# Performance work log

Measured on AMD Instinct MI355X. Metric: run time of the kernel, lower is better.

Reference implementation:

```python
import jax, jax.numpy as jnp
import numpy as np

N_NODES = 100000
N_EDGES = 1600000
DIMS = [128, 128, 128, 64]  # in, h1, h2, out


def setup_inputs() -> dict:
    key = jax.random.key(0)
    ks = jax.random.split(key, 12)
    inp = {
        "x": jax.random.normal(ks[0], (N_NODES, DIMS[0]), dtype=jnp.float32),
        "edge_index": jax.random.randint(ks[1], (2, N_EDGES), 0, N_NODES, dtype=jnp.int64),
        "edge_weights": jax.random.uniform(ks[2], (N_EDGES,), dtype=jnp.float32),
    }
    for i in range(3):
        inp[f"W{i+1}"] = jax.random.normal(ks[3 + 2 * i], (DIMS[i], DIMS[i + 1]), dtype=jnp.float32) * 0.05
        inp[f"b{i+1}"] = jax.random.normal(ks[4 + 2 * i], (DIMS[i + 1],), dtype=jnp.float32) * 0.01
    return inp


def gcn_conv(x, src, dst, w, W, b, n_nodes):
    # PyG GCNConv: linear transform, symmetric gcn_norm with self-loops (weight 1), scatter-add, bias.
    xw = x @ W                                            # [N, out]
    deg = jax.ops.segment_sum(w, dst, num_segments=n_nodes) + 1.0  # self-loop weight 1
    dinv = jnp.where(deg > 0, jax.lax.rsqrt(deg), 0.0)    # deg^{-1/2}
    norm = dinv[src] * w * dinv[dst]                      # [E]
    out = jax.ops.segment_sum(norm[:, None] * xw[src], dst, num_segments=n_nodes)
    out = out + (dinv * dinv)[:, None] * xw               # self-loop message
    return out + b


def reference(x, edge_index, edge_weights, W1, b1, W2, b2, W3, b3):
    src, dst = edge_index[0], edge_index[1]
    n = x.shape[0]
    # layer 1: GCNConv -> dropout(p=0) -> relu
    h = jax.nn.relu(gcn_conv(x, src, dst, edge_weights, W1, b1, n))
    # layer 2
    h = jax.nn.relu(gcn_conv(h, src, dst, edge_weights, W2, b2, n))
    # layer 3: activation 'none' -> Identity
    h = gcn_conv(h, src, dst, edge_weights, W3, b3, n)
    return h
```

## Files before the change

### kernel.cpp

```cpp
#include <hip/hip_runtime.h>
#include <hip/hip_fp16.h>
#include <math.h>


typedef __bf16 bf16x8 __attribute__((ext_vector_type(8)));
typedef float f32x4 __attribute__((ext_vector_type(4)));

union BF8 {
  unsigned short u[8];
  uint4 q;
  bf16x8 v;
};

union H8 {
  uint4 q;
  __half2 h2[4];
};

__device__ __forceinline__ unsigned short rne_bf16(float f) {
  unsigned u = __float_as_uint(f);
  u += 0x7fff + ((u >> 16) & 1);
  return (unsigned short)(u >> 16);
}
__device__ __forceinline__ float bf16_to_f(unsigned short h) {
  return __uint_as_float((unsigned)h << 16);
}

__device__ __forceinline__ void gemm_body_slice(const float* __restrict__ A,
    const float* __restrict__ W, int ldw, int col0,
    unsigned short* __restrict__ Ch, int ldc, int M, int bid) {
  constexpr int NF = 4;
  __shared__ __align__(16) unsigned short WT[2][64][128];
  const int t = threadIdx.x;
#pragma unroll
  for (int it = 0; it < 4; ++it) {
    int n = t & 63;
    int kc = it * 4 + (t >> 6);
    int k0 = kc * 8;
    BF8 hh, ll;
#pragma unroll
    for (int j = 0; j < 8; ++j) {
      float w = W[(size_t)(k0 + j) * ldw + col0 + n];
      unsigned short hb = rne_bf16(w);
      hh.u[j] = hb;
      ll.u[j] = rne_bf16(w - bf16_to_f(hb));
    }
    int kk = k0 ^ ((n & 7) << 3);
    *(uint4*)&WT[0][n][kk] = hh.q;
    *(uint4*)&WT[1][n][kk] = ll.q;
  }
  __syncthreads();

  const int wv = t >> 6;
  const int l = t & 63;
  const int lr = l & 15;
  const int lg = l >> 4;
  const int arow_i = bid * 64 + wv * 16 + lr;
  const bool rv = arow_i < M;
  const float* arow = A + (size_t)arow_i * 128;

  f32x4 acc[NF] = {};
  float4 p0 = make_float4(0.f, 0.f, 0.f, 0.f), p1 = p0;
  if (rv) {
    p0 = *(const float4*)&arow[lg * 8];
    p1 = *(const float4*)&arow[lg * 8 + 4];
  }
#pragma unroll 1
  for (int ks = 0; ks < 4; ++ks) {
    int nkb = ((ks < 3) ? (ks + 1) * 32 : ks * 32) + lg * 8;
    float4 q0 = make_float4(0.f, 0.f, 0.f, 0.f), q1 = q0;
    if (rv) {
      q0 = *(const float4*)&arow[nkb];
      q1 = *(const float4*)&arow[nkb + 4];
    }
    float av[8] = {p0.x, p0.y, p0.z, p0.w, p1.x, p1.y, p1.z, p1.w};
    BF8 ah, al;
#pragma unroll
    for (int j = 0; j < 8; ++j) {
      unsigned short hb = rne_bf16(av[j]);
      ah.u[j] = hb;
      al.u[j] = rne_bf16(av[j] - bf16_to_f(hb));
    }
    int kidx = ks * 32 + lg * 8;
    BF8 bh[NF], bl[NF];
#pragma unroll
    for (int nf = 0; nf < NF; ++nf) {
      int n = nf * 16 + lr;
      int kk = kidx ^ ((n & 7) << 3);
      bh[nf].q = *(const uint4*)&WT[0][n][kk];
      bl[nf].q = *(const uint4*)&WT[1][n][kk];
    }
#pragma unroll
    for (int nf = 0; nf < NF; ++nf) {
      acc[nf] = __builtin_amdgcn_mfma_f32_16x16x32_bf16(ah.v, bh[nf].v, acc[nf], 0, 0, 0);
      acc[nf] = __builtin_amdgcn_mfma_f32_16x16x32_bf16(al.v, bh[nf].v, acc[nf], 0, 0, 0);
      acc[nf] = __builtin_amdgcn_mfma_f32_16x16x32_bf16(ah.v, bl[nf].v, acc[nf], 0, 0, 0);
    }
    p0 = q0; p1 = q1;
  }
  const int orow0 = bid * 64 + wv * 16 + lg * 4;
#pragma unroll
  for (int j = 0; j < 4; ++j) {
    int orow = orow0 + j;
    if (orow < M) {
      unsigned short* hr = Ch + (size_t)orow * ldc + col0;
#pragma unroll
      for (int nf = 0; nf < NF; ++nf)
        hr[nf * 16 + lr] = __half_as_ushort(__float2half(acc[nf][j]));
    }
  }
}

__global__ __launch_bounds__(256) void pre_gemm_fused_kernel(
    const float* __restrict__ x, const float* __restrict__ W1,
    unsigned short* __restrict__ Ch, int M,
    const int* __restrict__ ei, const float* __restrict__ ew,
    unsigned long long* __restrict__ packed, int* __restrict__ rank,
    int E, int edgeBlocks) {
  if ((int)blockIdx.x < edgeBlocks) {
    int e = blockIdx.x * 256 + threadIdx.x;
    if (e >= E) return;
    int d = ei[E + e];
    unsigned wfix = (unsigned)__float2uint_rn(ew[e] * 16777216.0f);
    unsigned long long inc = (1ULL << 32) | (unsigned long long)wfix;
    unsigned long long old = atomicAdd(&packed[d], inc);
    rank[e] = (int)(old >> 32);
  } else {
    int g = blockIdx.x - edgeBlocks;
    gemm_body_slice(x, W1, 128, (g & 1) * 64, Ch, 128, M, g >> 1);
  }
}

template <int NCOL>
__global__ __launch_bounds__(256) void gemm_mfma_kernel(
    const unsigned short* __restrict__ Ah, const float* __restrict__ W,
    unsigned short* __restrict__ Ch, int M) {
  constexpr int NF = NCOL / 16;
  __shared__ __align__(16) unsigned short WT[2][NCOL][128];
  const int t = threadIdx.x;
  constexpr int KC_PER_IT = 256 / NCOL;
#pragma unroll
  for (int it = 0; it < 16 / KC_PER_IT; ++it) {
    int n = t % NCOL;
    int kc = it * KC_PER_IT + t / NCOL;
    int k0 = kc * 8;
    BF8 hh, ll;
#pragma unroll
    for (int j = 0; j < 8; ++j) {
      float w = W[(size_t)(k0 + j) * NCOL + n];
      unsigned short hb = rne_bf16(w);
      hh.u[j] = hb;
      ll.u[j] = rne_bf16(w - bf16_to_f(hb));
    }
    int kk = k0 ^ ((n & 7) << 3);
    *(uint4*)&WT[0][n][kk] = hh.q;
    *(uint4*)&WT[1][n][kk] = ll.q;
  }
  __syncthreads();

  const int wv = t >> 6;
  const int l = t & 63;
  const int lr = l & 15;
  const int lg = l >> 4;
  const int arow_i = blockIdx.x * 64 + wv * 16 + lr;
  const bool rv = arow_i < M;
  const unsigned short* arowh = Ah + (size_t)arow_i * 128;

  f32x4 acc[NF] = {};
  uint4 ph = make_uint4(0, 0, 0, 0);
  if (rv) ph = *(const uint4*)&arowh[lg * 8];
#pragma unroll 1
  for (int ks = 0; ks < 4; ++ks) {
    int nkb = ((ks < 3) ? (ks + 1) * 32 : ks * 32) + lg * 8;
    uint4 qh = make_uint4(0, 0, 0, 0);
    if (rv) qh = *(const uint4*)&arowh[nkb];
    float av[8];
    {
      H8 uu; uu.q = ph;
#pragma unroll
      for (int j = 0; j < 4; ++j) {
        float2 f = __half22float2(uu.h2[j]);
        av[j * 2] = f.x; av[j * 2 + 1] = f.y;
      }
    }
    BF8 ah, al;
#pragma unroll
    for (int j = 0; j < 8; ++j) {
      unsigned short hb = rne_bf16(av[j]);
      ah.u[j] = hb;
      al.u[j] = rne_bf16(av[j] - bf16_to_f(hb));
    }
    int kidx = ks * 32 + lg * 8;
    BF8 bh[NF], bl[NF];
#pragma unroll
    for (int nf = 0; nf < NF; ++nf) {
      int n = nf * 16 + lr;
      int kk = kidx ^ ((n & 7) << 3);
      bh[nf].q = *(const uint4*)&WT[0][n][kk];
      bl[nf].q = *(const uint4*)&WT[1][n][kk];
    }
#pragma unroll
    for (int nf = 0; nf < NF; ++nf) {
      acc[nf] = __builtin_amdgcn_mfma_f32_16x16x32_bf16(ah.v, bh[nf].v, acc[nf], 0, 0, 0);
      acc[nf] = __builtin_amdgcn_mfma_f32_16x16x32_bf16(al.v, bh[nf].v, acc[nf], 0, 0, 0);
      acc[nf] = __builtin_amdgcn_mfma_f32_16x16x32_bf16(ah.v, bl[nf].v, acc[nf], 0, 0, 0);
    }
    ph = qh;
  }
  const int orow0 = blockIdx.x * 64 + wv * 16 + lg * 4;
#pragma unroll
  for (int j = 0; j < 4; ++j) {
    int orow = orow0 + j;
    if (orow < M) {
      unsigned short* hr = Ch + (size_t)orow * NCOL;
#pragma unroll
      for (int nf = 0; nf < NF; ++nf)
        hr[nf * 16 + lr] = __half_as_ushort(__float2half(acc[nf][j]));
    }
  }
}

__global__ __launch_bounds__(1024) void scanA(const unsigned long long* __restrict__ packed,
    int* __restrict__ row_ptr, int* __restrict__ partials,
    float* __restrict__ dinv, int n) {
  __shared__ int sd[1024];
  int t = threadIdx.x;
  int i = blockIdx.x * 1024 + t;
  unsigned long long pv = (i < n) ? packed[i] : 0ULL;
  int v = (int)(pv >> 32);
  if (i < n) {
    float deg = 1.0f + (float)(unsigned)(pv & 0xffffffffULL) * (1.0f / 16777216.0f);
    dinv[i] = 1.0f / sqrtf(deg);
  }
  sd[t] = v;
  __syncthreads();
  for (int off = 1; off < 1024; off <<= 1) {
    int u = (t >= off) ? sd[t - off] : 0;
    __syncthreads();
    sd[t] += u;
    __syncthreads();
  }
  int incl = sd[t];
  if (i < n) row_ptr[i] = incl - v;
  if (t == 1023) partials[blockIdx.x] = incl;
}

__global__ __launch_bounds__(128) void scanB(int* partials, int nb) {
  __shared__ int sd[128];
  int t = threadIdx.x;
  int v = (t < nb) ? partials[t] : 0;
  sd[t] = v;
  __syncthreads();
  for (int off = 1; off < 128; off <<= 1) {
    int u = (t >= off) ? sd[t - off] : 0;
    __syncthreads();
    sd[t] += u;
    __syncthreads();
  }
  int incl = sd[t];
  partials[t] = incl - v;
  if (t == nb - 1) partials[255] = incl;
}

__global__ __launch_bounds__(1024) void scanC(int* row_ptr, const int* __restrict__ partials, int n) {
  int i = blockIdx.x * 1024 + threadIdx.x;
  if (i < n) row_ptr[i] += partials[blockIdx.x];
  if (i == 0) row_ptr[n] = partials[255];
}

__global__ __launch_bounds__(256) void fill_kernel(const int* __restrict__ ei,
    const float* __restrict__ ew, const float* __restrict__ dinv,
    const int* __restrict__ row_ptr, const int* __restrict__ rank,
    int2* __restrict__ epair, int E) {
  int e = blockIdx.x * 256 + threadIdx.x;
  if (e >= E) return;
  int s = ei[e], d = ei[E + e];
  float nw = dinv[s] * ew[e] * dinv[d];
  int p = row_ptr[d] + rank[e];
  epair[p] = make_int2(s, __float_as_int(nw));
}

template <int F, bool RELU, bool OUTF16>
__global__ __launch_bounds__(256) void agg_kernel(const unsigned short* __restrict__ xwh,
    const int* __restrict__ row_ptr, const int2* __restrict__ epair,
    const float* __restrict__ dinv, const float* __restrict__ bias,
    void* __restrict__ out, int Nn) {
  constexpr int LPN = F / 8;
  int t = blockIdx.x * 256 + threadIdx.x;
  int node = t / LPN;
  int lane = t % LPN;
  if (node >= Nn) return;
  const uint4* xh = (const uint4*)xwh;
  int start = row_ptr[node];
  int end = row_ptr[node + 1];
  float a0[8] = {}, a1[8] = {};
  int p = start;
  for (; p + 4 <= end; p += 4) {
    int2 e0 = epair[p];
    int2 e1 = epair[p + 1];
    int2 e2 = epair[p + 2];
    int2 e3 = epair[p + 3];
    H8 u0, u1, u2, u3;
    u0.q = xh[(size_t)e0.x * LPN + lane];
    u1.q = xh[(size_t)e1.x * LPN + lane];
    u2.q = xh[(size_t)e2.x * LPN + lane];
    u3.q = xh[(size_t)e3.x * LPN + lane];
    float n0 = __int_as_float(e0.y), n1 = __int_as_float(e1.y);
    float n2 = __int_as_float(e2.y), n3 = __int_as_float(e3.y);
#pragma unroll
    for (int j = 0; j < 4; ++j) {
      float2 f0 = __half22float2(u0.h2[j]);
      float2 f1 = __half22float2(u1.h2[j]);
      float2 f2 = __half22float2(u2.h2[j]);
      float2 f3 = __half22float2(u3.h2[j]);
      a0[j * 2]     = fmaf(n0, f0.x, a0[j * 2]);
      a0[j * 2 + 1] = fmaf(n0, f0.y, a0[j * 2 + 1]);
      a1[j * 2]     = fmaf(n1, f1.x, a1[j * 2]);
      a1[j * 2 + 1] = fmaf(n1, f1.y, a1[j * 2 + 1]);
      a0[j * 2]     = fmaf(n2, f2.x, a0[j * 2]);
      a0[j * 2 + 1] = fmaf(n2, f2.y, a0[j * 2 + 1]);
      a1[j * 2]     = fmaf(n3, f3.x, a1[j * 2]);
      a1[j * 2 + 1] = fmaf(n3, f3.y, a1[j * 2 + 1]);
    }
  }
  for (; p < end; ++p) {
    int2 pr = epair[p];
    float nw = __int_as_float(pr.y);
    H8 u; u.q = xh[(size_t)pr.x * LPN + lane];
#pragma unroll
    for (int j = 0; j < 4; ++j) {
      float2 f = __half22float2(u.h2[j]);
      a0[j * 2]     = fmaf(nw, f.x, a0[j * 2]);
      a0[j * 2 + 1] = fmaf(nw, f.y, a0[j * 2 + 1]);
    }
  }
  float di = dinv[node];
  float sw = di * di;
  H8 su; su.q = xh[(size_t)node * LPN + lane];
#pragma unroll
  for (int j = 0; j < 4; ++j) {
    float2 f = __half22float2(su.h2[j]);
    a0[j * 2]     = fmaf(sw, f.x, a0[j * 2]);
    a0[j * 2 + 1] = fmaf(sw, f.y, a0[j * 2 + 1]);
  }
  float4 b0 = ((const float4*)bias)[lane * 2];
  float4 b1 = ((const float4*)bias)[lane * 2 + 1];
  float o[8];
  o[0] = a0[0] + a1[0] + b0.x; o[1] = a0[1] + a1[1] + b0.y;
  o[2] = a0[2] + a1[2] + b0.z; o[3] = a0[3] + a1[3] + b0.w;
  o[4] = a0[4] + a1[4] + b1.x; o[5] = a0[5] + a1[5] + b1.y;
  o[6] = a0[6] + a1[6] + b1.z; o[7] = a0[7] + a1[7] + b1.w;
  if (RELU) {
#pragma unroll
    for (int j = 0; j < 8; ++j) o[j] = fmaxf(o[j], 0.f);
  }
  if constexpr (OUTF16) {
    H8 w;
#pragma unroll
    for (int j = 0; j < 4; ++j)
      w.h2[j] = __float22half2_rn(make_float2(o[j * 2], o[j * 2 + 1]));
    ((uint4*)out)[(size_t)node * LPN + lane] = w.q;
  } else {
    float4* of = (float4*)out + (size_t)node * LPN * 2 + lane * 2;
    of[0] = make_float4(o[0], o[1], o[2], o[3]);
    of[1] = make_float4(o[4], o[5], o[6], o[7]);
  }
}

extern "C" void kernel_launch(void* const* d_in, const int* in_sizes, int n_in,
                              void* d_out, int out_size, void* d_ws, size_t ws_size,
                              hipStream_t stream) {
  const float* x  = (const float*)d_in[0];
  const int*   ei = (const int*)d_in[1];
  const float* ew = (const float*)d_in[2];
  const float* W1 = (const float*)d_in[3];
  const float* b1 = (const float*)d_in[4];
  const float* W2 = (const float*)d_in[5];
  const float* b2 = (const float*)d_in[6];
  const float* W3 = (const float*)d_in[7];
  const float* b3 = (const float*)d_in[8];

  const int N = in_sizes[0] / 128;
  const int E = in_sizes[2];

  char* ws = (char*)d_ws;
  size_t off = 0;
  auto carve = [&](size_t bytes) -> void* {
    void* p = ws + off;
    off += (bytes + 255) & ~(size_t)255;
    return p;
  };
  unsigned long long* packed = (unsigned long long*)carve((size_t)N * 8);
  int*   rank    = (int*)carve((size_t)E * 4);
  float* dinv    = (float*)carve((size_t)N * 4);
  int*   row_ptr = (int*)carve((size_t)(N + 1) * 4);
  int*   parts   = (int*)carve(256 * 4);
  int2*  epair   = (int2*)carve((size_t)E * 8);
  unsigned short* bufH = (unsigned short*)carve((size_t)N * 128 * 2);
  unsigned short* bufI = (unsigned short*)carve((size_t)N * 128 * 2);
  (void)ws_size; (void)n_in; (void)out_size;

  const int nThreads = 256;
  int gE  = (E + nThreads - 1) / nThreads;
  int nb  = (N + 1023) / 1024;
  const int gMM = (N + 63) / 64;
  int gAgg128 = (N * 16 + nThreads - 1) / nThreads;
  int gAgg64  = (N * 8 + nThreads - 1) / nThreads;

  hipMemsetAsync(packed, 0, (size_t)N * 8, stream);
  pre_gemm_fused_kernel<<<gE + 2 * gMM, nThreads, 0, stream>>>(
      x, W1, bufH, N, ei, ew, packed, rank, E, gE);

  scanA<<<nb, 1024, 0, stream>>>(packed, row_ptr, parts, dinv, N);
  scanB<<<1, 128, 0, stream>>>(parts, nb);
  scanC<<<nb, 1024, 0, stream>>>(row_ptr, parts, N);
  fill_kernel<<<gE, nThreads, 0, stream>>>(ei, ew, dinv, row_ptr, rank, epair, E);

  agg_kernel<128, true, true><<<gAgg128, nThreads, 0, stream>>>(bufH, row_ptr, epair, dinv, b1, bufI, N);

  gemm_mfma_kernel<128><<<gMM, nThreads, 0, stream>>>(bufI, W2, bufH, N);
  agg_kernel<128, true, true><<<gAgg128, nThreads, 0, stream>>>(bufH, row_ptr, epair, dinv, b2, bufI, N);

  gemm_mfma_kernel<64><<<gMM, nThreads, 0, stream>>>(bufI, W3, bufH, N);
  agg_kernel<64, false, false><<<gAgg64, nThreads, 0, stream>>>(bufH, row_ptr, epair, dinv, b3, d_out, N);
}
```

Before: 341.4 us.

## Process two 16-row tiles per wave in MFMA GEMMs to reuse B fragments

```diff
diff --git a/kernel.cpp b/kernel.cpp
--- a/kernel.cpp
+++ b/kernel.cpp
@@ -24,6 +24,15 @@
 }
 __device__ __forceinline__ float bf16_to_f(unsigned short h) {
   return __uint_as_float((unsigned)h << 16);
+}
+
+__device__ __forceinline__ void split_f32_to_bf(const float* av, BF8& ah, BF8& al) {
+#pragma unroll
+  for (int j = 0; j < 8; ++j) {
+    unsigned short hb = rne_bf16(av[j]);
+    ah.u[j] = hb;
+    al.u[j] = rne_bf16(av[j] - bf16_to_f(hb));
+  }
 }
 
 __device__ __forceinline__ void gemm_body_slice(const float* __restrict__ A,
@@ -55,58 +64,60 @@
   const int l = t & 63;
   const int lr = l & 15;
   const int lg = l >> 4;
-  const int arow_i = bid * 64 + wv * 16 + lr;
-  const bool rv = arow_i < M;
-  const float* arow = A + (size_t)arow_i * 128;
-
-  f32x4 acc[NF] = {};
-  float4 p0 = make_float4(0.f, 0.f, 0.f, 0.f), p1 = p0;
-  if (rv) {
-    p0 = *(const float4*)&arow[lg * 8];
-    p1 = *(const float4*)&arow[lg * 8 + 4];
-  }
+  const int r0 = bid * 128 + wv * 32 + lr;
+  const int r1 = r0 + 16;
+  const bool v0 = r0 < M, v1 = r1 < M;
+  const float* a0p = A + (size_t)r0 * 128;
+  const float* a1p = A + (size_t)r1 * 128;
+
+  f32x4 acc0[NF] = {}, acc1[NF] = {};
+  float4 p00 = make_float4(0.f, 0.f, 0.f, 0.f), p01 = p00, p10 = p00, p11 = p00;
+  if (v0) { p00 = *(const float4*)&a0p[lg * 8]; p01 = *(const float4*)&a0p[lg * 8 + 4]; }
+  if (v1) { p10 = *(const float4*)&a1p[lg * 8]; p11 = *(const float4*)&a1p[lg * 8 + 4]; }
 #pragma unroll 1
   for (int ks = 0; ks < 4; ++ks) {
     int nkb = ((ks < 3) ? (ks + 1) * 32 : ks * 32) + lg * 8;
-    float4 q0 = make_float4(0.f, 0.f, 0.f, 0.f), q1 = q0;
-    if (rv) {
-      q0 = *(const float4*)&arow[nkb];
-      q1 = *(const float4*)&arow[nkb + 4];
-    }
-    float av[8] = {p0.x, p0.y, p0.z, p0.w, p1.x, p1.y, p1.z, p1.w};
-    BF8 ah, al;
-#pragma unroll
-    for (int j = 0; j < 8; ++j) {
-      unsigned short hb = rne_bf16(av[j]);
-      ah.u[j] = hb;
-      al.u[j] = rne_bf16(av[j] - bf16_to_f(hb));
-    }
+    float4 q00 = make_float4(0.f, 0.f, 0.f, 0.f), q01 = q00, q10 = q00, q11 = q00;
+    if (v0) { q00 = *(const float4*)&a0p[nkb]; q01 = *(const float4*)&a0p[nkb + 4]; }
+    if (v1) { q10 = *(const float4*)&a1p[nkb]; q11 = *(const float4*)&a1p[nkb + 4]; }
+    float av0[8] = {p00.x, p00.y, p00.z, p00.w, p01.x, p01.y, p01.z, p01.w};
+    float av1[8] = {p10.x, p10.y, p10.z, p10.w, p11.x, p11.y, p11.z, p11.w};
+    BF8 ah0, al0, ah1, al1;
+    split_f32_to_bf(av0, ah0, al0);
+    split_f32_to_bf(av1, ah1, al1);
     int kidx = ks * 32 + lg * 8;
-    BF8 bh[NF], bl[NF];
 #pragma unroll
     for (int nf = 0; nf < NF; ++nf) {
       int n = nf * 16 + lr;
       int kk = kidx ^ ((n & 7) << 3);
-      bh[nf].q = *(const uint4*)&WT[0][n][kk];
-      bl[nf].q = *(const uint4*)&WT[1][n][kk];
-    }
-#pragma unroll
-    for (int nf = 0; nf < NF; ++nf) {
-      acc[nf] = __builtin_amdgcn_mfma_f32_16x16x32_bf16(ah.v, bh[nf].v, acc[nf], 0, 0, 0);
-      acc[nf] = __builtin_amdgcn_mfma_f32_16x16x32_bf16(al.v, bh[nf].v, acc[nf], 0, 0, 0);
-      acc[nf] = __builtin_amdgcn_mfma_f32_16x16x32_bf16(ah.v, bl[nf].v, acc[nf], 0, 0, 0);
-    }
-    p0 = q0; p1 = q1;
-  }
-  const int orow0 = bid * 64 + wv * 16 + lg * 4;
+      BF8 bh, bl;
+      bh.q = *(const uint4*)&WT[0][n][kk];
+      bl.q = *(const uint4*)&WT[1][n][kk];
+      acc0[nf] = __builtin_amdgcn_mfma_f32_16x16x32_bf16(ah0.v, bh.v, acc0[nf], 0, 0, 0);
+      acc0[nf] = __builtin_amdgcn_mfma_f32_16x16x32_bf16(al0.v, bh.v, acc0[nf], 0, 0, 0);
+      acc0[nf] = __builtin_amdgcn_mfma_f32_16x16x32_bf16(ah0.v, bl.v, acc0[nf], 0, 0, 0);
+      acc1[nf] = __builtin_amdgcn_mfma_f32_16x16x32_bf16(ah1.v, bh.v, acc1[nf], 0, 0, 0);
+      acc1[nf] = __builtin_amdgcn_mfma_f32_16x16x32_bf16(al1.v, bh.v, acc1[nf], 0, 0, 0);
+      acc1[nf] = __builtin_amdgcn_mfma_f32_16x16x32_bf16(ah1.v, bl.v, acc1[nf], 0, 0, 0);
+    }
+    p00 = q00; p01 = q01; p10 = q10; p11 = q11;
+  }
+  const int ob = bid * 128 + wv * 32 + lg * 4;
 #pragma unroll
   for (int j = 0; j < 4; ++j) {
-    int orow = orow0 + j;
+    int orow = ob + j;
     if (orow < M) {
       unsigned short* hr = Ch + (size_t)orow * ldc + col0;
 #pragma unroll
       for (int nf = 0; nf < NF; ++nf)
-        hr[nf * 16 + lr] = __half_as_ushort(__float2half(acc[nf][j]));
+        hr[nf * 16 + lr] = __half_as_ushort(__float2half(acc0[nf][j]));
+    }
+    int orow1 = ob + 16 + j;
+    if (orow1 < M) {
+      unsigned short* hr = Ch + (size_t)orow1 * ldc + col0;
+#pragma unroll
+      for (int nf = 0; nf < NF; ++nf)
+        hr[nf * 16 + lr] = __half_as_ushort(__float2half(acc1[nf][j]));
     }
   }
 }
@@ -162,60 +173,73 @@
   const int l = t & 63;
   const int lr = l & 15;
   const int lg = l >> 4;
-  const int arow_i = blockIdx.x * 64 + wv * 16 + lr;
-  const bool rv = arow_i < M;
-  const unsigned short* arowh = Ah + (size_t)arow_i * 128;
-
-  f32x4 acc[NF] = {};
-  uint4 ph = make_uint4(0, 0, 0, 0);
-  if (rv) ph = *(const uint4*)&arowh[lg * 8];
+  const int r0 = blockIdx.x * 128 + wv * 32 + lr;
+  const int r1 = r0 + 16;
+  const bool v0 = r0 < M, v1 = r1 < M;
+  const unsigned short* a0p = Ah + (size_t)r0 * 128;
+  const unsigned short* a1p = Ah + (size_t)r1 * 128;
+
+  f32x4 acc0[NF] = {}, acc1[NF] = {};
+  uint4 ph0 = make_uint4(0, 0, 0, 0), ph1 = ph0;
+  if (v0) ph0 = *(const uint4*)&a0p[lg * 8];
+  if (v1) ph1 = *(const uint4*)&a1p[lg * 8];
 #pragma unroll 1
   for (int ks = 0; ks < 4; ++ks) {
     int nkb = ((ks < 3) ? (ks + 1) * 32 : ks * 32) + lg * 8;
-    uint4 qh = make_uint4(0, 0, 0, 0);
-    if (rv) qh = *(const uint4*)&arowh[nkb];
-    float av[8];
+    uint4 qh0 = make_uint4(0, 0, 0, 0), qh1 = qh0;
+    if (v0) qh0 = *(const uint4*)&a0p[nkb];
+    if (v1) qh1 = *(const uint4*)&a1p[nkb];
+    float av0[8], av1[8];
     {
-      H8 uu; uu.q = ph;
+      H8 uu; uu.q = ph0;
 #pragma unroll
       for (int j = 0; j < 4; ++j) {
         float2 f = __half22float2(uu.h2[j]);
-        av[j * 2] = f.x; av[j * 2 + 1] = f.y;
+        av0[j * 2] = f.x; av0[j * 2 + 1] = f.y;
       }
-    }
-    BF8 ah, al;
-#pragma unroll
-    for (int j = 0; j < 8; ++j) {
-      unsigned short hb = rne_bf16(av[j]);
-      ah.u[j] = hb;
-      al.u[j] = rne_bf16(av[j] - bf16_to_f(hb));
-    }
+      uu.q = ph1;
+#pragma unroll
+      for (int j = 0; j < 4; ++j) {
+        float2 f = __half22float2(uu.h2[j]);
+        av1[j * 2] = f.x; av1[j * 2 + 1] = f.y;
+      }
+    }
+    BF8 ah0, al0, ah1, al1;
+    split_f32_to_bf(av0, ah0, al0);
+    split_f32_to_bf(av1, ah1, al1);
     int kidx = ks * 32 + lg * 8;
-    BF8 bh[NF], bl[NF];
 #pragma unroll
     for (int nf = 0; nf < NF; ++nf) {
       int n = nf * 16 + lr;
       int kk = kidx ^ ((n & 7) << 3);
-      bh[nf].q = *(const uint4*)&WT[0][n][kk];
-      bl[nf].q = *(const uint4*)&WT[1][n][kk];
-    }
-#pragma unroll
-    for (int nf = 0; nf < NF; ++nf) {
-      acc[nf] = __builtin_amdgcn_mfma_f32_16x16x32_bf16(ah.v, bh[nf].v, acc[nf], 0, 0, 0);
-      acc[nf] = __builtin_amdgcn_mfma_f32_16x16x32_bf16(al.v, bh[nf].v, acc[nf], 0, 0, 0);
-      acc[nf] = __builtin_amdgcn_mfma_f32_16x16x32_bf16(ah.v, bl[nf].v, acc[nf], 0, 0, 0);
-    }
-    ph = qh;
-  }
-  const int orow0 = blockIdx.x * 64 + wv * 16 + lg * 4;
+      BF8 bh, bl;
+      bh.q = *(const uint4*)&WT[0][n][kk];
+      bl.q = *(const uint4*)&WT[1][n][kk];
+      acc0[nf] = __builtin_amdgcn_mfma_f32_16x16x32_bf16(ah0.v, bh.v, acc0[nf], 0, 0, 0);
+      acc0[nf] = __builtin_amdgcn_mfma_f32_16x16x32_bf16(al0.v, bh.v, acc0[nf], 0, 0, 0);
+      acc0[nf] = __builtin_amdgcn_mfma_f32_16x16x32_bf16(ah0.v, bl.v, acc0[nf], 0, 0, 0);
+      acc1[nf] = __builtin_amdgcn_mfma_f32_16x16x32_bf16(ah1.v, bh.v, acc1[nf], 0, 0, 0);
+      acc1[nf] = __builtin_amdgcn_mfma_f32_16x16x32_bf16(al1.v, bh.v, acc1[nf], 0, 0, 0);
+      acc1[nf] = __builtin_amdgcn_mfma_f32_16x16x32_bf16(ah1.v, bl.v, acc1[nf], 0, 0, 0);
+    }
+    ph0 = qh0; ph1 = qh1;
+  }
+  const int ob = blockIdx.x * 128 + wv * 32 + lg * 4;
 #pragma unroll
   for (int j = 0; j < 4; ++j) {
-    int orow = orow0 + j;
+    int orow = ob + j;
     if (orow < M) {
       unsigned short* hr = Ch + (size_t)orow * NCOL;
 #pragma unroll
       for (int nf = 0; nf < NF; ++nf)
-        hr[nf * 16 + lr] = __half_as_ushort(__float2half(acc[nf][j]));
+        hr[nf * 16 + lr] = __half_as_ushort(__float2half(acc0[nf][j]));
+    }
+    int orow1 = ob + 16 + j;
+    if (orow1 < M) {
+      unsigned short* hr = Ch + (size_t)orow1 * NCOL;
+#pragma unroll
+      for (int nf = 0; nf < NF; ++nf)
+        hr[nf * 16 + lr] = __half_as_ushort(__float2half(acc1[nf][j]));
     }
   }
 }
@@ -403,7 +427,7 @@
   const int nThreads = 256;
   int gE  = (E + nThreads - 1) / nThreads;
   int nb  = (N + 1023) / 1024;
-  const int gMM = (N + 63) / 64;
+  const int gMM = (N + 127) / 128;
   int gAgg128 = (N * 16 + nThreads - 1) / nThreads;
   int gAgg64  = (N * 8 + nThreads - 1) / nThreads;
 
```

New measurement: 335.0 us (median of 2 runs). Within noise of the previous version (-1.9%).
